# Optimization experiments

Hardware: AMD Instinct MI355X
Metric: run time of the kernel (lower is better)

The kernel has to match this reference:

```python
import jax, jax.numpy as jnp
import numpy as np

HIDDEN = 1024
HEADS = 16
HEAD_DIM = HIDDEN // HEADS
B, T = 4, 2048


def setup_inputs() -> dict:
    key = jax.random.key(0)
    k_x, k_w1, k_b1, k_w2, k_b2 = jax.random.split(key, 5)
    lim1 = 1.0 / np.sqrt(HIDDEN)
    x = jax.random.normal(k_x, (B, T, HIDDEN), dtype=jnp.float32)
    # causal lower-triangular mask, broadcastable to [B, H, T, T]
    mask = jnp.tril(jnp.ones((T, T), dtype=jnp.int32))[None, None, :, :]
    # qkv_proj: Linear(HIDDEN, 3*HIDDEN); torch Linear: y = x @ W.T + b
    W_qkv = jax.random.uniform(k_w1, (3 * HIDDEN, HIDDEN), minval=-lim1, maxval=lim1, dtype=jnp.float32)
    b_qkv = jax.random.uniform(k_b1, (3 * HIDDEN,), minval=-lim1, maxval=lim1, dtype=jnp.float32)
    W_out = jax.random.uniform(k_w2, (HIDDEN, HIDDEN), minval=-lim1, maxval=lim1, dtype=jnp.float32)
    b_out = jax.random.uniform(k_b2, (HIDDEN,), minval=-lim1, maxval=lim1, dtype=jnp.float32)
    return {"x": x, "mask": mask, "W_qkv": W_qkv, "b_qkv": b_qkv, "W_out": W_out, "b_out": b_out}


def reference(x, mask, W_qkv, b_qkv, W_out, b_out):
    Bx, Tx, C = x.shape
    qkv = x @ W_qkv.T + b_qkv                      # [B, T, 3C]
    qkv = qkv.reshape(Bx, Tx, 3, HEADS, HEAD_DIM)
    qkv = jnp.transpose(qkv, (2, 0, 3, 1, 4))      # [3, B, H, T, Dh]
    Q, K, V = qkv[0], qkv[1], qkv[2]
    scale = 1.0 / np.sqrt(HEAD_DIM)
    scores = jnp.einsum('bhqd,bhkd->bhqk', Q, K) * scale  # [B, H, T, T]
    scores = jnp.where(mask == 0, -jnp.inf, scores)
    probs = jax.nn.softmax(scores, axis=-1)
    ctx = jnp.einsum('bhqk,bhkd->bhqd', probs, V)  # [B, H, T, Dh]
    ctx = jnp.transpose(ctx, (0, 2, 1, 3)).reshape(Bx, Tx, C)
    return ctx @ W_out.T + b_out
```

## Files before the change

### kernel.cpp

```cpp
#include <hip/hip_runtime.h>
#include <cstdint>
#include <cstddef>

#define B_ 4
#define T_ 2048
#define C_ 1024
#define H_ 16
#define D_ 64

typedef __attribute__((ext_vector_type(8))) __bf16 bf16x8;
typedef __attribute__((ext_vector_type(4))) float floatx4;

#define QSCL (0.125f * 1.44269504088896f)
#define FMAX 24.0f

__device__ __forceinline__ unsigned short f2bf(float f) {
  union { float f; unsigned int u; } v; v.f = f;
  unsigned int r = v.u + 0x7fffu + ((v.u >> 16) & 1u);
  return (unsigned short)(r >> 16);
}
__device__ __forceinline__ ushort4 pk4(float a, float b, float c, float d) {
  ushort4 u; u.x = f2bf(a); u.y = f2bf(b); u.z = f2bf(c); u.w = f2bf(d);
  return u;
}
__device__ __forceinline__ bf16x8 cvt8(float4 a, float4 b) {
  bf16x8 r;
  r[0] = a.x; r[1] = a.y; r[2] = a.z; r[3] = a.w;
  r[4] = b.x; r[5] = b.y; r[6] = b.z; r[7] = b.w;
  return r;
}
__device__ __forceinline__ ushort4 pk4c(float a, float b, float c, float d) {
  union { __bf16 b4[4]; ushort4 u; } w;
  w.b4[0] = (__bf16)a; w.b4[1] = (__bf16)b; w.b4[2] = (__bf16)c; w.b4[3] = (__bf16)d;
  return w.u;
}

__device__ __forceinline__ void gl_lds16(const void* g, void* l) {
  __builtin_amdgcn_global_load_lds(
      (const __attribute__((address_space(1))) unsigned int*)g,
      (__attribute__((address_space(3))) unsigned int*)l, 16, 0, 0);
}

__global__ __launch_bounds__(256)
void conv_bf16(const float* __restrict__ src, unsigned short* __restrict__ dst,
               int n8) {
  for (int i = blockIdx.x * 256 + threadIdx.x; i < n8; i += gridDim.x * 256) {
    const float4* s = (const float4*)src + 2 * (size_t)i;
    float4 a = s[0], b = s[1];
    ((bf16x8*)dst)[i] = cvt8(a, b);
  }
}

__global__ __launch_bounds__(256)
void conv_dual(const float* __restrict__ s1, unsigned short* __restrict__ d1, int n1,
               const float* __restrict__ s2, unsigned short* __restrict__ d2, int n2) {
  for (int i = blockIdx.x * 256 + threadIdx.x; i < n1 + n2; i += gridDim.x * 256) {
    const float4* sp; bf16x8* dp;
    if (i < n1) { sp = (const float4*)s1 + 2 * (size_t)i;       dp = (bf16x8*)d1 + i; }
    else { int j = i - n1; sp = (const float4*)s2 + 2 * (size_t)j; dp = (bf16x8*)d2 + j; }
    float4 a = sp[0], b = sp[1];
    *dp = cvt8(a, b);
  }
}

template<int EPI, int GATHER, int WBF>
__global__ __launch_bounds__(256, 3)
void gemm_bt(const unsigned short* __restrict__ Abf,
             const void* __restrict__ Wraw,
             const float* __restrict__ bias,
             float* __restrict__ out,
             unsigned short* __restrict__ qws,
             unsigned short* __restrict__ kws,
             unsigned short* __restrict__ vtws)
{
  alignas(16) __shared__ unsigned short As[128 * 64];
  alignas(16) __shared__ unsigned short Bs[WBF ? 128 * 64 : 128 * 72];
  const int tid  = threadIdx.x;
  const int lane = tid & 63;
  const int wid  = tid >> 6;
  const int col  = lane & 15;
  const int quad = lane >> 4;
  const int wm = (wid >> 1) << 6;
  const int wn = (wid & 1) << 6;
  const int bm = blockIdx.y << 7;
  const int bn = blockIdx.x << 7;

  const float* Wf          = (const float*)Wraw;
  const unsigned short* Wb = (const unsigned short*)Wraw;

  const int r0 = tid >> 3;
  const int c0 = tid & 7;

  floatx4 acc[4][4];
#pragma unroll
  for (int i = 0; i < 4; ++i)
#pragma unroll
    for (int j = 0; j < 4; ++j)
      acc[i][j] = (floatx4){0.f, 0.f, 0.f, 0.f};

  for (int k0 = 0; k0 < 1024; k0 += 64) {
    __syncthreads();
#pragma unroll
    for (int s = 0; s < 4; ++s) {
      const int row  = (s << 5) + r0;
      const int colE = ((c0 ^ (row & 7)) << 3);
      const unsigned short* gsrc;
      if (GATHER) {
        const int m = bm + row;
        const int b = m >> 11, t = m & 2047;
        const int h = k0 >> 6;
        gsrc = Abf + ((((size_t)(b * 16 + h) << 11) + t) << 6) + colE;
      } else {
        gsrc = Abf + (size_t)(bm + row) * 1024 + k0 + colE;
      }
      gl_lds16(gsrc, (char*)As + (s << 12) + (wid << 10));
    }
    if (WBF) {
#pragma unroll
      for (int s = 0; s < 4; ++s) {
        const int row  = (s << 5) + r0;
        const int colE = ((c0 ^ (row & 7)) << 3);
        const unsigned short* gsrc = Wb + (size_t)(bn + row) * 1024 + k0 + colE;
        gl_lds16(gsrc, (char*)Bs + (s << 12) + (wid << 10));
      }
    } else {
#pragma unroll
      for (int s = 0; s < 4; ++s) {
        const int row = (s << 5) + r0;
        const int kc  = c0 << 3;
        const float* wsrc = &Wf[(size_t)(bn + row) * 1024 + k0 + kc];
        float4 w0 = *(const float4*)wsrc;
        float4 w1 = *(const float4*)(wsrc + 4);
        *(bf16x8*)&Bs[row * 72 + kc] = cvt8(w0, w1);
      }
    }
    __syncthreads();
#pragma unroll
    for (int kk = 0; kk < 64; kk += 32) {
      bf16x8 af[4], bfr[4];
#pragma unroll
      for (int i = 0; i < 4; ++i) {
        const int r = wm + i * 16 + col;
        af[i] = *(const bf16x8*)&As[(r << 6) + ((kk + quad * 8) ^ ((r & 7) << 3))];
      }
#pragma unroll
      for (int j = 0; j < 4; ++j) {
        const int r = wn + j * 16 + col;
        if (WBF)
          bfr[j] = *(const bf16x8*)&Bs[(r << 6) + ((kk + quad * 8) ^ ((r & 7) << 3))];
        else
          bfr[j] = *(const bf16x8*)&Bs[r * 72 + kk + quad * 8];
      }
#pragma unroll
      for (int i = 0; i < 4; ++i)
#pragma unroll
        for (int j = 0; j < 4; ++j)
          acc[i][j] = __builtin_amdgcn_mfma_f32_16x16x32_bf16(af[i], bfr[j], acc[i][j], 0, 0, 0);
    }
  }

#pragma unroll
  for (int i = 0; i < 4; ++i) {
    const int row = bm + wm + i * 16 + quad * 4;
#pragma unroll
    for (int j = 0; j < 4; ++j) {
      const int n  = bn + wn + j * 16 + col;
      const float bv = bias[n];
      float v[4];
#pragma unroll
      for (int r = 0; r < 4; ++r) v[r] = acc[i][j][r] + bv;

      if (EPI == 1) {
#pragma unroll
        for (int r = 0; r < 4; ++r)
          out[(size_t)(row + r) * 1024 + n] = v[r];
      } else {
        const int s   = n >> 10;
        const int rem = n & 1023;
        const int h   = rem >> 6;
        const int d   = rem & 63;
        const int b   = row >> 11;
        const int t   = row & 2047;
        const size_t bh = (size_t)(b * H_ + h);
        if (s == 0) {
#pragma unroll
          for (int r = 0; r < 4; ++r)
            qws[(bh * T_ + t + r) * D_ + d] = f2bf(v[r] * QSCL);
        } else if (s == 1) {
#pragma unroll
          for (int r = 0; r < 4; ++r)
            kws[(bh * T_ + t + r) * D_ + d] = f2bf(v[r]);
        } else {
          *(ushort4*)&vtws[(bh * D_ + d) * T_ + t] = pk4(v[0], v[1], v[2], v[3]);
        }
      }
    }
  }
}

__global__ __launch_bounds__(256, 2)
void attn_causal(unsigned short* __restrict__ qws,
                 const unsigned short* __restrict__ kws,
                 const unsigned short* __restrict__ vtws)
{
  alignas(16) __shared__ unsigned short Ks[2][64 * 64];
  alignas(16) __shared__ unsigned short Vs[2][64 * 64];
  alignas(16) __shared__ unsigned short Ps[4][2][16][72];
  const int tid  = threadIdx.x;
  const int lane = tid & 63;
  const int wid  = tid >> 6;
  const int col  = lane & 15;
  const int quad = lane >> 4;

  const int bh = blockIdx.x & 63;
  const int pr = blockIdx.x >> 6;

  const unsigned short* Kp  = kws + (size_t)bh * T_ * D_;
  const unsigned short* Vtp = vtws + (size_t)bh * D_ * T_;

  bf16x8 vones;
#pragma unroll
  for (int i = 0; i < 8; ++i) vones[i] = (__bf16)1.0f;

  const int srow8 = lane >> 3;
  const int swz   = ((lane & 7) ^ srow8) << 3;

#define STAGE(kt_, b_)                                                        \
  do {                                                                        \
    _Pragma("unroll") for (int c2 = 0; c2 < 2; ++c2) {                        \
      const int cb = wid + (c2 << 2);                   \
      gl_lds16(Kp + ((size_t)(((kt_) << 6) + (cb << 3) + srow8) << 6) + swz,  \
               (char*)&Ks[b_][0] + (cb << 10));                               \
      gl_lds16(Vtp + ((size_t)((cb << 3) + srow8) << 11) + ((kt_) << 6) + swz,\
               (char*)&Vs[b_][0] + (cb << 10));                               \
    }                                                                         \
  } while (0)

#pragma unroll
  for (int half = 0; half < 2; ++half) {
    const int band = (half == 0) ? pr : (15 - pr);
    const int nk   = (band << 1) + 2;
    const int q0   = (band << 7) + (wid << 5);
    unsigned short* Qp = qws + ((size_t)bh * T_ + q0) * D_;

    bf16x8 bq[2][2];
#pragma unroll
    for (int h = 0; h < 2; ++h) {
      bq[h][0] = *(const bf16x8*)&Qp[(h * 16 + col) * D_ + quad * 8];
      bq[h][1] = *(const bf16x8*)&Qp[(h * 16 + col) * D_ + 32 + quad * 8];
    }

    floatx4 o[2][4], ol[2];
#pragma unroll
    for (int h = 0; h < 2; ++h) {
      ol[h] = (floatx4){0.f, 0.f, 0.f, 0.f};
#pragma unroll
      for (int j = 0; j < 4; ++j) o[h][j] = (floatx4){0.f, 0.f, 0.f, 0.f};
    }

    STAGE(0, 0);
    __syncthreads();

    for (int kt = 0; kt < nk; ++kt) {
      const int buf = kt & 1;
      if (kt + 1 < nk) STAGE(kt + 1, buf ^ 1);

      const unsigned short* Kb = &Ks[buf][0];
      bf16x8 kA[4], kB[4];
#pragma unroll
      for (int g = 0; g < 4; ++g) {
        const int r = g * 16 + col;
        kA[g] = *(const bf16x8*)&Kb[(r << 6) + ((quad ^ (col & 7)) << 3)];
        kB[g] = *(const bf16x8*)&Kb[(r << 6) + (((quad | 4) ^ (col & 7)) << 3)];
      }

      floatx4 s[2][4];
      __builtin_amdgcn_s_setprio(1);
#pragma unroll
      for (int h = 0; h < 2; ++h)
#pragma unroll
        for (int g = 0; g < 4; ++g) {
          s[h][g] = (floatx4){-FMAX, -FMAX, -FMAX, -FMAX};
          s[h][g] = __builtin_amdgcn_mfma_f32_16x16x32_bf16(kA[g], bq[h][0], s[h][g], 0, 0, 0);
          s[h][g] = __builtin_amdgcn_mfma_f32_16x16x32_bf16(kB[g], bq[h][1], s[h][g], 0, 0, 0);
        }
      __builtin_amdgcn_s_setprio(0);

      if (kt >= nk - 2) {
#pragma unroll
        for (int h = 0; h < 2; ++h) {
          const int lim = q0 - (kt << 6) + (h << 4) + col;
#pragma unroll
          for (int g = 0; g < 4; ++g)
#pragma unroll
            for (int r = 0; r < 4; ++r)
              if (g * 16 + quad * 4 + r > lim) s[h][g][r] = -1e30f;
        }
      }

#pragma unroll
      for (int h = 0; h < 2; ++h)
#pragma unroll
        for (int g = 0; g < 4; ++g)
#pragma unroll
          for (int r = 0; r < 4; ++r)
            s[h][g][r] = exp2f(s[h][g][r]);

#pragma unroll
      for (int h = 0; h < 2; ++h)
#pragma unroll
        for (int g = 0; g < 4; ++g)
          *(ushort4*)&Ps[wid][h][col][g * 16 + quad * 4] =
              pk4c(s[h][g][0], s[h][g][1], s[h][g][2], s[h][g][3]);
      asm volatile("s_waitcnt lgkmcnt(0)" ::: "memory");

      const unsigned short* Vb = &Vs[buf][0];
      bf16x8 vA[4], vB[4];
#pragma unroll
      for (int j = 0; j < 4; ++j) {
        const int r = j * 16 + col;
        vA[j] = *(const bf16x8*)&Vb[(r << 6) + ((quad ^ (col & 7)) << 3)];
        vB[j] = *(const bf16x8*)&Vb[(r << 6) + (((quad | 4) ^ (col & 7)) << 3)];
      }

      __builtin_amdgcn_s_setprio(1);
#pragma unroll
      for (int h = 0; h < 2; ++h) {
        const bf16x8 ap0 = *(const bf16x8*)&Ps[wid][h][col][quad * 8];
        const bf16x8 ap1 = *(const bf16x8*)&Ps[wid][h][col][32 + quad * 8];
#pragma unroll
        for (int j = 0; j < 4; ++j) {
          o[h][j] = __builtin_amdgcn_mfma_f32_16x16x32_bf16(ap0, vA[j], o[h][j], 0, 0, 0);
          o[h][j] = __builtin_amdgcn_mfma_f32_16x16x32_bf16(ap1, vB[j], o[h][j], 0, 0, 0);
        }
        ol[h] = __builtin_amdgcn_mfma_f32_16x16x32_bf16(ap0, vones, ol[h], 0, 0, 0);
        ol[h] = __builtin_amdgcn_mfma_f32_16x16x32_bf16(ap1, vones, ol[h], 0, 0, 0);
      }
      __builtin_amdgcn_s_setprio(0);

      __syncthreads();
    }

#pragma unroll
    for (int h = 0; h < 2; ++h) {
      float lr[4];
#pragma unroll
      for (int r = 0; r < 4; ++r) lr[r] = 1.0f / ol[h][r];
#pragma unroll
      for (int j = 0; j < 4; ++j)
#pragma unroll
        for (int r = 0; r < 4; ++r)
          Qp[(size_t)(h * 16 + quad * 4 + r) * D_ + j * 16 + col] =
              f2bf(o[h][j][r] * lr[r]);
    }
  }
#undef STAGE
}

extern "C" void kernel_launch(void* const* d_in, const int* in_sizes, int n_in,
                              void* d_out, int out_size, void* d_ws, size_t ws_size,
                              hipStream_t stream) {
  const float* x     = (const float*)d_in[0];
  const float* W_qkv = (const float*)d_in[2];
  const float* b_qkv = (const float*)d_in[3];
  const float* W_out = (const float*)d_in[4];
  const float* b_out = (const float*)d_in[5];
  float* out = (float*)d_out;

  const size_t per = (size_t)B_ * H_ * T_ * D_;
  unsigned short* qws  = (unsigned short*)d_ws;
  unsigned short* vtws = qws + per;
  unsigned short* kws  = (unsigned short*)d_out;
  unsigned short* xbf  = kws + per;

  const bool bigws = ws_size >= (size_t)38 * 1024 * 1024;
  unsigned short* wqbf = vtws + per;

  if (bigws) {
    conv_dual<<<dim3(2048), 256, 0, stream>>>(x, xbf, (int)(per >> 3),
                                              W_qkv, wqbf, (3 * C_ * C_) >> 3);
    gemm_bt<0, 0, 1><<<dim3(3072 / 128, 8192 / 128), 256, 0, stream>>>(
        xbf, (const void*)wqbf, b_qkv, nullptr, qws, kws, vtws);
  } else {
    conv_bf16<<<dim3(2048), 256, 0, stream>>>(x, xbf, (int)(per >> 3));
    gemm_bt<0, 0, 0><<<dim3(3072 / 128, 8192 / 128), 256, 0, stream>>>(
        xbf, (const void*)W_qkv, b_qkv, nullptr, qws, kws, vtws);
  }

  attn_causal<<<dim3(8 * 64), 256, 0, stream>>>(qws, kws, vtws);

  conv_bf16<<<dim3(512), 256, 0, stream>>>(W_out, vtws, (C_ * C_) >> 3);

  gemm_bt<1, 1, 1><<<dim3(1024 / 128, 8192 / 128), 256, 0, stream>>>(
      qws, (const void*)vtws, b_out, out, nullptr, nullptr, nullptr);
}
```

Before: 263.4 us.

## Split causal attention into one band per block and fold W_out conversion upfront

The attention kernel now gives each block a single 128-row query band, heaviest bands first, instead of pairing a light and a heavy band per block. This doubles the grid and raises the occupancy hint to 3 blocks per CU. When the workspace is large enough, W_out is converted to bf16 together with x and W_qkv in one three-way conversion launch, which removes a separate launch before the output GEMM. The trade-off is more, unequal blocks that rely on the hardware scheduler to balance the causal triangle, and a tighter register budget.

Measured after the change: 265.8 us. Within noise of the previous version (+0.9%).

```diff
diff --git a/kernel.cpp b/kernel.cpp
--- a/kernel.cpp
+++ b/kernel.cpp
@@ -52,12 +52,14 @@
 }
 
 __global__ __launch_bounds__(256)
-void conv_dual(const float* __restrict__ s1, unsigned short* __restrict__ d1, int n1,
-               const float* __restrict__ s2, unsigned short* __restrict__ d2, int n2) {
-  for (int i = blockIdx.x * 256 + threadIdx.x; i < n1 + n2; i += gridDim.x * 256) {
+void conv_tri(const float* __restrict__ s1, unsigned short* __restrict__ d1, int n1,
+              const float* __restrict__ s2, unsigned short* __restrict__ d2, int n2,
+              const float* __restrict__ s3, unsigned short* __restrict__ d3, int n3) {
+  for (int i = blockIdx.x * 256 + threadIdx.x; i < n1 + n2 + n3; i += gridDim.x * 256) {
     const float4* sp; bf16x8* dp;
-    if (i < n1) { sp = (const float4*)s1 + 2 * (size_t)i;       dp = (bf16x8*)d1 + i; }
-    else { int j = i - n1; sp = (const float4*)s2 + 2 * (size_t)j; dp = (bf16x8*)d2 + j; }
+    if (i < n1)           { sp = (const float4*)s1 + 2 * (size_t)i;       dp = (bf16x8*)d1 + i; }
+    else if (i < n1 + n2) { int j = i - n1;      sp = (const float4*)s2 + 2 * (size_t)j; dp = (bf16x8*)d2 + j; }
+    else                  { int j = i - n1 - n2; sp = (const float4*)s3 + 2 * (size_t)j; dp = (bf16x8*)d3 + j; }
     float4 a = sp[0], b = sp[1];
     *dp = cvt8(a, b);
   }
@@ -198,7 +200,7 @@
   }
 }
 
-__global__ __launch_bounds__(256, 2)
+__global__ __launch_bounds__(256, 3)
 void attn_causal(unsigned short* __restrict__ qws,
                  const unsigned short* __restrict__ kws,
                  const unsigned short* __restrict__ vtws)
@@ -212,8 +214,8 @@
   const int col  = lane & 15;
   const int quad = lane >> 4;
 
-  const int bh = blockIdx.x & 63;
-  const int pr = blockIdx.x >> 6;
+  const int bh   = blockIdx.x & 63;
+  const int band = 15 - (blockIdx.x >> 6);
 
   const unsigned short* Kp  = kws + (size_t)bh * T_ * D_;
   const unsigned short* Vtp = vtws + (size_t)bh * D_ * T_;
@@ -236,123 +238,119 @@
     }                                                                         \
   } while (0)
 
-#pragma unroll
-  for (int half = 0; half < 2; ++half) {
-    const int band = (half == 0) ? pr : (15 - pr);
-    const int nk   = (band << 1) + 2;
-    const int q0   = (band << 7) + (wid << 5);
-    unsigned short* Qp = qws + ((size_t)bh * T_ + q0) * D_;
-
-    bf16x8 bq[2][2];
+  const int nk = (band << 1) + 2;
+  const int q0 = (band << 7) + (wid << 5);
+  unsigned short* Qp = qws + ((size_t)bh * T_ + q0) * D_;
+
+  bf16x8 bq[2][2];
+#pragma unroll
+  for (int h = 0; h < 2; ++h) {
+    bq[h][0] = *(const bf16x8*)&Qp[(h * 16 + col) * D_ + quad * 8];
+    bq[h][1] = *(const bf16x8*)&Qp[(h * 16 + col) * D_ + 32 + quad * 8];
+  }
+
+  floatx4 o[2][4], ol[2];
+#pragma unroll
+  for (int h = 0; h < 2; ++h) {
+    ol[h] = (floatx4){0.f, 0.f, 0.f, 0.f};
+#pragma unroll
+    for (int j = 0; j < 4; ++j) o[h][j] = (floatx4){0.f, 0.f, 0.f, 0.f};
+  }
+
+  STAGE(0, 0);
+  __syncthreads();
+
+  for (int kt = 0; kt < nk; ++kt) {
+    const int buf = kt & 1;
+    if (kt + 1 < nk) STAGE(kt + 1, buf ^ 1);
+
+    const unsigned short* Kb = &Ks[buf][0];
+    bf16x8 kA[4], kB[4];
+#pragma unroll
+    for (int g = 0; g < 4; ++g) {
+      const int r = g * 16 + col;
+      kA[g] = *(const bf16x8*)&Kb[(r << 6) + ((quad ^ (col & 7)) << 3)];
+      kB[g] = *(const bf16x8*)&Kb[(r << 6) + (((quad | 4) ^ (col & 7)) << 3)];
+    }
+
+    floatx4 s[2][4];
+    __builtin_amdgcn_s_setprio(1);
+#pragma unroll
+    for (int h = 0; h < 2; ++h)
+#pragma unroll
+      for (int g = 0; g < 4; ++g) {
+        s[h][g] = (floatx4){-FMAX, -FMAX, -FMAX, -FMAX};
+        s[h][g] = __builtin_amdgcn_mfma_f32_16x16x32_bf16(kA[g], bq[h][0], s[h][g], 0, 0, 0);
+        s[h][g] = __builtin_amdgcn_mfma_f32_16x16x32_bf16(kB[g], bq[h][1], s[h][g], 0, 0, 0);
+      }
+    __builtin_amdgcn_s_setprio(0);
+
+    if (kt >= nk - 2) {
+#pragma unroll
+      for (int h = 0; h < 2; ++h) {
+        const int lim = q0 - (kt << 6) + (h << 4) + col;
+#pragma unroll
+        for (int g = 0; g < 4; ++g)
+#pragma unroll
+          for (int r = 0; r < 4; ++r)
+            if (g * 16 + quad * 4 + r > lim) s[h][g][r] = -1e30f;
+      }
+    }
+
+#pragma unroll
+    for (int h = 0; h < 2; ++h)
+#pragma unroll
+      for (int g = 0; g < 4; ++g)
+#pragma unroll
+        for (int r = 0; r < 4; ++r)
+          s[h][g][r] = exp2f(s[h][g][r]);
+
+#pragma unroll
+    for (int h = 0; h < 2; ++h)
+#pragma unroll
+      for (int g = 0; g < 4; ++g)
+        *(ushort4*)&Ps[wid][h][col][g * 16 + quad * 4] =
+            pk4c(s[h][g][0], s[h][g][1], s[h][g][2], s[h][g][3]);
+    asm volatile("s_waitcnt lgkmcnt(0)" ::: "memory");
+
+    const unsigned short* Vb = &Vs[buf][0];
+    bf16x8 vA[4], vB[4];
+#pragma unroll
+    for (int j = 0; j < 4; ++j) {
+      const int r = j * 16 + col;
+      vA[j] = *(const bf16x8*)&Vb[(r << 6) + ((quad ^ (col & 7)) << 3)];
+      vB[j] = *(const bf16x8*)&Vb[(r << 6) + (((quad | 4) ^ (col & 7)) << 3)];
+    }
+
+    __builtin_amdgcn_s_setprio(1);
 #pragma unroll
     for (int h = 0; h < 2; ++h) {
-      bq[h][0] = *(const bf16x8*)&Qp[(h * 16 + col) * D_ + quad * 8];
-      bq[h][1] = *(const bf16x8*)&Qp[(h * 16 + col) * D_ + 32 + quad * 8];
-    }
-
-    floatx4 o[2][4], ol[2];
-#pragma unroll
-    for (int h = 0; h < 2; ++h) {
-      ol[h] = (floatx4){0.f, 0.f, 0.f, 0.f};
-#pragma unroll
-      for (int j = 0; j < 4; ++j) o[h][j] = (floatx4){0.f, 0.f, 0.f, 0.f};
-    }
-
-    STAGE(0, 0);
+      const bf16x8 ap0 = *(const bf16x8*)&Ps[wid][h][col][quad * 8];
+      const bf16x8 ap1 = *(const bf16x8*)&Ps[wid][h][col][32 + quad * 8];
+#pragma unroll
+      for (int j = 0; j < 4; ++j) {
+        o[h][j] = __builtin_amdgcn_mfma_f32_16x16x32_bf16(ap0, vA[j], o[h][j], 0, 0, 0);
+        o[h][j] = __builtin_amdgcn_mfma_f32_16x16x32_bf16(ap1, vB[j], o[h][j], 0, 0, 0);
+      }
+      ol[h] = __builtin_amdgcn_mfma_f32_16x16x32_bf16(ap0, vones, ol[h], 0, 0, 0);
+      ol[h] = __builtin_amdgcn_mfma_f32_16x16x32_bf16(ap1, vones, ol[h], 0, 0, 0);
+    }
+    __builtin_amdgcn_s_setprio(0);
+
     __syncthreads();
-
-    for (int kt = 0; kt < nk; ++kt) {
-      const int buf = kt & 1;
-      if (kt + 1 < nk) STAGE(kt + 1, buf ^ 1);
-
-      const unsigned short* Kb = &Ks[buf][0];
-      bf16x8 kA[4], kB[4];
-#pragma unroll
-      for (int g = 0; g < 4; ++g) {
-        const int r = g * 16 + col;
-        kA[g] = *(const bf16x8*)&Kb[(r << 6) + ((quad ^ (col & 7)) << 3)];
-        kB[g] = *(const bf16x8*)&Kb[(r << 6) + (((quad | 4) ^ (col & 7)) << 3)];
-      }
-
-      floatx4 s[2][4];
-      __builtin_amdgcn_s_setprio(1);
-#pragma unroll
-      for (int h = 0; h < 2; ++h)
-#pragma unroll
-        for (int g = 0; g < 4; ++g) {
-          s[h][g] = (floatx4){-FMAX, -FMAX, -FMAX, -FMAX};
-          s[h][g] = __builtin_amdgcn_mfma_f32_16x16x32_bf16(kA[g], bq[h][0], s[h][g], 0, 0, 0);
-          s[h][g] = __builtin_amdgcn_mfma_f32_16x16x32_bf16(kB[g], bq[h][1], s[h][g], 0, 0, 0);
-        }
-      __builtin_amdgcn_s_setprio(0);
-
-      if (kt >= nk - 2) {
-#pragma unroll
-        for (int h = 0; h < 2; ++h) {
-          const int lim = q0 - (kt << 6) + (h << 4) + col;
-#pragma unroll
-          for (int g = 0; g < 4; ++g)
-#pragma unroll
-            for (int r = 0; r < 4; ++r)
-              if (g * 16 + quad * 4 + r > lim) s[h][g][r] = -1e30f;
-        }
-      }
-
-#pragma unroll
-      for (int h = 0; h < 2; ++h)
-#pragma unroll
-        for (int g = 0; g < 4; ++g)
-#pragma unroll
-          for (int r = 0; r < 4; ++r)
-            s[h][g][r] = exp2f(s[h][g][r]);
-
-#pragma unroll
-      for (int h = 0; h < 2; ++h)
-#pragma unroll
-        for (int g = 0; g < 4; ++g)
-          *(ushort4*)&Ps[wid][h][col][g * 16 + quad * 4] =
-              pk4c(s[h][g][0], s[h][g][1], s[h][g][2], s[h][g][3]);
-      asm volatile("s_waitcnt lgkmcnt(0)" ::: "memory");
-
-      const unsigned short* Vb = &Vs[buf][0];
-      bf16x8 vA[4], vB[4];
-#pragma unroll
-      for (int j = 0; j < 4; ++j) {
-        const int r = j * 16 + col;
-        vA[j] = *(const bf16x8*)&Vb[(r << 6) + ((quad ^ (col & 7)) << 3)];
-        vB[j] = *(const bf16x8*)&Vb[(r << 6) + (((quad | 4) ^ (col & 7)) << 3)];
-      }
-
-      __builtin_amdgcn_s_setprio(1);
-#pragma unroll
-      for (int h = 0; h < 2; ++h) {
-        const bf16x8 ap0 = *(const bf16x8*)&Ps[wid][h][col][quad * 8];
-        const bf16x8 ap1 = *(const bf16x8*)&Ps[wid][h][col][32 + quad * 8];
-#pragma unroll
-        for (int j = 0; j < 4; ++j) {
-          o[h][j] = __builtin_amdgcn_mfma_f32_16x16x32_bf16(ap0, vA[j], o[h][j], 0, 0, 0);
-          o[h][j] = __builtin_amdgcn_mfma_f32_16x16x32_bf16(ap1, vB[j], o[h][j], 0, 0, 0);
-        }
-        ol[h] = __builtin_amdgcn_mfma_f32_16x16x32_bf16(ap0, vones, ol[h], 0, 0, 0);
-        ol[h] = __builtin_amdgcn_mfma_f32_16x16x32_bf16(ap1, vones, ol[h], 0, 0, 0);
-      }
-      __builtin_amdgcn_s_setprio(0);
-
-      __syncthreads();
-    }
-
-#pragma unroll
-    for (int h = 0; h < 2; ++h) {
-      float lr[4];
-#pragma unroll
-      for (int r = 0; r < 4; ++r) lr[r] = 1.0f / ol[h][r];
-#pragma unroll
-      for (int j = 0; j < 4; ++j)
-#pragma unroll
-        for (int r = 0; r < 4; ++r)
-          Qp[(size_t)(h * 16 + quad * 4 + r) * D_ + j * 16 + col] =
-              f2bf(o[h][j][r] * lr[r]);
-    }
+  }
+
+#pragma unroll
+  for (int h = 0; h < 2; ++h) {
+    float lr[4];
+#pragma unroll
+    for (int r = 0; r < 4; ++r) lr[r] = 1.0f / ol[h][r];
+#pragma unroll
+    for (int j = 0; j < 4; ++j)
+#pragma unroll
+      for (int r = 0; r < 4; ++r)
+        Qp[(size_t)(h * 16 + quad * 4 + r) * D_ + j * 16 + col] =
+            f2bf(o[h][j][r] * lr[r]);
   }
 #undef STAGE
 }
@@ -373,12 +371,23 @@
   unsigned short* kws  = (unsigned short*)d_out;
   unsigned short* xbf  = kws + per;
 
-  const bool bigws = ws_size >= (size_t)38 * 1024 * 1024;
+  const bool bigws  = ws_size >= (size_t)38 * 1024 * 1024;
+  const bool hugews = ws_size >= (size_t)40 * 1024 * 1024;
   unsigned short* wqbf = vtws + per;
-
-  if (bigws) {
-    conv_dual<<<dim3(2048), 256, 0, stream>>>(x, xbf, (int)(per >> 3),
-                                              W_qkv, wqbf, (3 * C_ * C_) >> 3);
+  unsigned short* wobf = wqbf + (size_t)3 * C_ * C_;
+
+  if (hugews) {
+    conv_tri<<<dim3(2048), 256, 0, stream>>>(
+        x, xbf, (int)(per >> 3),
+        W_qkv, wqbf, (3 * C_ * C_) >> 3,
+        W_out, wobf, (C_ * C_) >> 3);
+    gemm_bt<0, 0, 1><<<dim3(3072 / 128, 8192 / 128), 256, 0, stream>>>(
+        xbf, (const void*)wqbf, b_qkv, nullptr, qws, kws, vtws);
+  } else if (bigws) {
+    conv_tri<<<dim3(2048), 256, 0, stream>>>(
+        x, xbf, (int)(per >> 3),
+        W_qkv, wqbf, (3 * C_ * C_) >> 3,
+        nullptr, nullptr, 0);
     gemm_bt<0, 0, 1><<<dim3(3072 / 128, 8192 / 128), 256, 0, stream>>>(
         xbf, (const void*)wqbf, b_qkv, nullptr, qws, kws, vtws);
   } else {
@@ -387,10 +396,14 @@
         xbf, (const void*)W_qkv, b_qkv, nullptr, qws, kws, vtws);
   }
 
-  attn_causal<<<dim3(8 * 64), 256, 0, stream>>>(qws, kws, vtws);
-
-  conv_bf16<<<dim3(512), 256, 0, stream>>>(W_out, vtws, (C_ * C_) >> 3);
-
-  gemm_bt<1, 1, 1><<<dim3(1024 / 128, 8192 / 128), 256, 0, stream>>>(
-      qws, (const void*)vtws, b_out, out, nullptr, nullptr, nullptr);
-}
+  attn_causal<<<dim3(16 * 64), 256, 0, stream>>>(qws, kws, vtws);
+
+  if (hugews) {
+    gemm_bt<1, 1, 1><<<dim3(1024 / 128, 8192 / 128), 256, 0, stream>>>(
+        qws, (const void*)wobf, b_out, out, nullptr, nullptr, nullptr);
+  } else {
+    conv_bf16<<<dim3(512), 256, 0, stream>>>(W_out, vtws, (C_ * C_) >> 3);
+    gemm_bt<1, 1, 1><<<dim3(1024 / 128, 8192 / 128), 256, 0, stream>>>(
+        qws, (const void*)vtws, b_out, out, nullptr, nullptr, nullptr);
+  }
+}
```
